# Optimization experiments

Measured on AMD Instinct MI355X. Metric: run time of the kernel, lower is better.

The kernel has to match this reference:

```python
import jax, jax.numpy as jnp
import numpy as np

B, T, IN, H, OUT = 4096, 28, 28, 1024, 10


def setup_inputs() -> dict:
    key = jax.random.key(0)
    ks = jax.random.split(key, 6)
    s_ih = 1.0 / np.sqrt(IN)
    s_h = 1.0 / np.sqrt(H)
    return {
        "x": jax.random.normal(ks[0], (B, T, IN), dtype=jnp.float32),
        "W_ih": jax.random.uniform(ks[1], (IN, 4 * H), jnp.float32, -s_ih, s_ih),
        "W_hh": jax.random.uniform(ks[2], (H, 4 * H), jnp.float32, -s_h, s_h),
        "b": jax.random.uniform(ks[3], (4 * H,), jnp.float32, -s_h, s_h),
        "Wc": jax.random.uniform(ks[4], (H, OUT), jnp.float32, -s_h, s_h),
        "bc": jax.random.uniform(ks[5], (OUT,), jnp.float32, -s_h, s_h),
    }


def _lstm_last_hidden(x, W_ih, W_hh, b):
    # Precompute input projections for all timesteps: [T, B, 4H]
    xg = jnp.einsum('bti,ig->tbg', x, W_ih) + b
    h0 = jnp.zeros((x.shape[0], W_hh.shape[0]), x.dtype)
    c0 = jnp.zeros_like(h0)

    def step(carry, xg_t):
        h, c = carry
        gates = xg_t + h @ W_hh  # [B, 4H]
        i, f, g, o = jnp.split(gates, 4, axis=-1)
        i = jax.nn.sigmoid(i)
        f = jax.nn.sigmoid(f)
        g = jnp.tanh(g)
        o = jax.nn.sigmoid(o)
        c = f * c + i * g
        h = o * jnp.tanh(c)
        return (h, c), None

    (h, _), _ = jax.lax.scan(step, (h0, c0), xg)
    return h


def reference(x, W_ih, W_hh, b, Wc, bc):
    h = _lstm_last_hidden(x, W_ih, W_hh, b)
    # dropout is identity at inference (eval mode)
    return h @ Wc + bc
```

## Files before the change

kernel.cpp:

```cpp
#include <hip/hip_runtime.h>
#include <hip/hip_fp16.h>
#include <stdint.h>

#define GLOBAL_AS __attribute__((address_space(1)))
#define LDS_AS    __attribute__((address_space(3)))

typedef __attribute__((ext_vector_type(8))) short  short8;
typedef __attribute__((ext_vector_type(4))) float  floatx4;

static constexpr int B_   = 4096;
static constexpr int T_   = 28;
static constexpr int IN_  = 28;
static constexpr int H_   = 1024;
static constexpr int G4_  = 4096;
static constexpr int OUT_ = 10;
static constexpr int NT_  = 16;

__device__ __forceinline__ float bf2f(unsigned short u) {
  union { uint32_t i; float f; } v; v.i = ((uint32_t)u) << 16; return v.f;
}
__device__ __forceinline__ unsigned short f2bf(float f) {
  union { float f; uint32_t i; } v; v.f = f;
  uint32_t x = v.i;
  uint32_t lsb = (x >> 16) & 1u;
  x += 0x7fffu + lsb;
  return (unsigned short)(x >> 16);
}
__device__ __forceinline__ float sigm(float x) {
  return __builtin_amdgcn_rcpf(1.f + __builtin_amdgcn_exp2f(-1.4426950408889634f * x));
}
__device__ __forceinline__ float tanh_f(float x) {
  return 1.f - 2.f * __builtin_amdgcn_rcpf(1.f + __builtin_amdgcn_exp2f(2.8853900817779268f * x));
}
__device__ __forceinline__ void stage16(const unsigned short* g, unsigned short* l) {
  __builtin_amdgcn_global_load_lds(
      (const GLOBAL_AS uint32_t*)g, (LDS_AS uint32_t*)l, 16, 0, 0);
}

__global__ __launch_bounds__(256) void conv_x_kernel(const float* __restrict__ x,
                                                     unsigned short* __restrict__ xb) {
  int row = blockIdx.x * 256 + threadIdx.x;
  int t  = row >> 12;
  int bb = row & 4095;
  const float* src = x + (bb * T_ + t) * IN_;
  unsigned short* dst = xb + row * 32;
#pragma unroll
  for (int k = 0; k < IN_; ++k) dst[k] = f2bf(src[k]);
  dst[28] = 0; dst[29] = 0; dst[30] = 0; dst[31] = 0;
}

__global__ __launch_bounds__(256) void perm_whh_kernel(const float* __restrict__ whh,
                                                       unsigned short* __restrict__ wp) {
  __shared__ float lds[64][17];
  int g64  = blockIdx.x >> 2;
  int gate = blockIdx.x & 3;
  int oc0  = gate * H_ + g64 * 16;
  int n0   = g64 * 64 + gate * 16;
  int tid  = threadIdx.x;
  for (int kc = 0; kc < 16; ++kc) {
    int k0 = kc * 64;
    __syncthreads();
#pragma unroll
    for (int e = 0; e < 4; ++e) {
      int idx = e * 256 + tid;
      int k = idx >> 4, cc = idx & 15;
      lds[k][cc] = whh[(k0 + k) * G4_ + oc0 + cc];
    }
    __syncthreads();
#pragma unroll
    for (int e = 0; e < 4; ++e) {
      int idx = e * 256 + tid;
      int n = idx >> 6, kk = idx & 63;
      wp[(n0 + n) * H_ + k0 + kk] = f2bf(lds[kk][n]);
    }
  }
}

__global__ __launch_bounds__(256) void perm_wih_kernel(const float* __restrict__ wih,
                                                       unsigned short* __restrict__ wip) {
  __shared__ float lds[28][17];
  int g64  = blockIdx.x >> 2;
  int gate = blockIdx.x & 3;
  int oc0  = gate * H_ + g64 * 16;
  int n0   = g64 * 64 + gate * 16;
  int tid  = threadIdx.x;
  for (int idx = tid; idx < 448; idx += 256) {
    int k = idx >> 4, cc = idx & 15;
    lds[k][cc] = wih[k * G4_ + oc0 + cc];
  }
  __syncthreads();
#pragma unroll
  for (int e = 0; e < 2; ++e) {
    int idx = e * 256 + tid;
    int n = idx >> 5, kk = idx & 31;
    wip[(n0 + n) * 32 + kk] = (kk < IN_) ? f2bf(lds[kk][n]) : (unsigned short)0;
  }
}

__global__ __launch_bounds__(512, 4) void lstm_step_kernel(
    const unsigned short* __restrict__ hprev,
    const unsigned short* __restrict__ wp,
    const unsigned short* __restrict__ xbt,
    const unsigned short* __restrict__ wip,
    const float* __restrict__ bias,
    unsigned short* __restrict__ cst,
    unsigned short* __restrict__ hnext,
    int first) {
  __shared__ __align__(16) unsigned short lds[24576];

  const int tid = threadIdx.x;
  const int w   = tid >> 6;
  const int l   = tid & 63;
  const int wm  = w >> 1;
  const int wn  = w & 1;
  const int lc  = l & 15;
  const int lk  = l >> 4;

  const int hid = blockIdx.x;
  const int xcd = hid & 7, q = hid >> 3;
  const int bx  = (xcd & 1) * 8 + (q & 7);
  const int by  = (xcd >> 1) * 8 + (q >> 3);
  const int m0  = bx * 256;
  const int n0  = by * 128;

  const int swz  = (lc & 7) << 4;
  const int swzx = (lc & 3) << 4;

  const int r8  = tid >> 3;
  const int c8  = (tid & 7) * 8;
  const int c8s = c8 ^ ((r8 & 7) * 8);
  const int rx   = tid >> 2;
  const int cx8s = ((tid & 3) * 8) ^ ((rx & 3) * 8);

  auto stageA = [&](int kt, int i) {
    stage16(hprev + (size_t)(m0 + i * 64 + r8) * H_ + kt * 64 + c8s,
            lds + i * 4096 + tid * 8);
  };
  auto stageB = [&](int kt, int j) {
    stage16(wp + (size_t)(n0 + j * 64 + r8) * H_ + kt * 64 + c8s,
            lds + 16384 + j * 4096 + tid * 8);
  };
  auto stageXA = [&](int half) {
    stage16(xbt + (size_t)(m0 + half * 128 + rx) * 32 + cx8s,
            lds + half * 4096 + tid * 8);
  };
  auto stageXB = [&]() {
    stage16(wip + (size_t)(n0 + rx) * 32 + cx8s,
            lds + 8192 + tid * 8);
  };
  auto ldsr = [&](int byteoff) -> short8 {
    return *reinterpret_cast<const short8*>(reinterpret_cast<const char*>(lds) + byteoff);
  };

  floatx4 acc[4][4];
#pragma unroll
  for (int i = 0; i < 4; ++i)
#pragma unroll
    for (int j = 0; j < 4; ++j) acc[i][j] = (floatx4){0.f, 0.f, 0.f, 0.f};

  short8 a[4][2];
  short8 b[2][2];

#define LOAD_A                                                                       \
  _Pragma("unroll") for (int m_ = 0; m_ < 4; ++m_)                                   \
  _Pragma("unroll") for (int k_ = 0; k_ < 2; ++k_)                                   \
    a[m_][k_] = ldsr((wm * 64 + m_ * 16 + lc) * 128 + ((k_ * 64 + lk * 16) ^ swz));

#define LOAD_B(P)                                                                    \
  _Pragma("unroll") for (int n_ = 0; n_ < 2; ++n_)                                   \
  _Pragma("unroll") for (int k_ = 0; k_ < 2; ++k_)                                   \
    b[n_][k_] = ldsr(32768 + (wn * 64 + ((P) * 2 + n_) * 16 + lc) * 128 +            \
                     ((k_ * 64 + lk * 16) ^ swz));

#define MFMA_P(P)                                                                    \
  __builtin_amdgcn_s_setprio(1);                                                     \
  _Pragma("unroll") for (int m_ = 0; m_ < 4; ++m_)                                   \
  _Pragma("unroll") for (int n_ = 0; n_ < 2; ++n_)                                   \
  _Pragma("unroll") for (int k_ = 0; k_ < 2; ++k_)                                   \
    acc[m_][(P) * 2 + n_] = __builtin_amdgcn_mfma_f32_16x16x32_bf16(                 \
        a[m_][k_], b[n_][k_], acc[m_][(P) * 2 + n_], 0, 0, 0);                       \
  __builtin_amdgcn_s_setprio(0);

#define BAR_ONLY                                                                     \
  __builtin_amdgcn_sched_barrier(0);                                                 \
  __builtin_amdgcn_s_barrier();                                                      \
  __builtin_amdgcn_sched_barrier(0);

#define BAR_VM0                                                                      \
  __builtin_amdgcn_sched_barrier(0);                                                 \
  asm volatile("s_waitcnt vmcnt(0)" ::: "memory");                                   \
  __builtin_amdgcn_s_barrier();                                                      \
  __builtin_amdgcn_sched_barrier(0);

  stageXA(0); stageXA(1); stageXB();
  BAR_VM0
  {
    short8 xb4[4];
#pragma unroll
    for (int nf = 0; nf < 4; ++nf)
      xb4[nf] = ldsr(16384 + (wn * 64 + nf * 16 + lc) * 64 + ((lk * 16) ^ swzx));
    __builtin_amdgcn_s_setprio(1);
#pragma unroll
    for (int mf = 0; mf < 4; ++mf) {
      short8 xa = ldsr((wm * 64 + mf * 16 + lc) * 64 + ((lk * 16) ^ swzx));
#pragma unroll
      for (int nf = 0; nf < 4; ++nf)
        acc[mf][nf] = __builtin_amdgcn_mfma_f32_16x16x32_bf16(xa, xb4[nf], acc[mf][nf], 0, 0, 0);
    }
    __builtin_amdgcn_s_setprio(0);
  }

  if (!first) {
    BAR_ONLY
#pragma unroll
    for (int i = 0; i < 4; ++i) stageA(0, i);
    stageB(0, 0); stageB(0, 1);
    BAR_VM0
    for (int kt = 0; kt < NT_; ++kt) {
      LOAD_A
      LOAD_B(0)
      MFMA_P(0)
      LOAD_B(1)
      MFMA_P(1)
      if (kt + 1 < NT_) {
        BAR_ONLY
#pragma unroll
        for (int i = 0; i < 4; ++i) stageA(kt + 1, i);
        stageB(kt + 1, 0); stageB(kt + 1, 1);
        BAR_VM0
      }
    }
  }

  const int jj  = (by * 2 + wn) * 16 + lc;
  const float bi  = bias[jj];
  const float bf_ = bias[H_ + jj];
  const float bg_ = bias[2 * H_ + jj];
  const float bo_ = bias[3 * H_ + jj];
#pragma unroll
  for (int mf = 0; mf < 4; ++mf) {
    const int rbase = m0 + wm * 64 + mf * 16 + lk * 4;
#pragma unroll
    for (int r = 0; r < 4; ++r) {
      const size_t idx = (size_t)(rbase + r) * H_ + jj;
      float ig = sigm(acc[mf][0][r] + bi);
      float fg = sigm(acc[mf][1][r] + bf_);
      float gg = tanh_f(acc[mf][2][r] + bg_);
      float og = sigm(acc[mf][3][r] + bo_);
      float cp = first ? 0.f : __half2float(__ushort_as_half(cst[idx]));
      float cn = fg * cp + ig * gg;
      cst[idx] = __half_as_ushort(__float2half(cn));
      hnext[idx] = f2bf(og * tanh_f(cn));
    }
  }
#undef LOAD_A
#undef LOAD_B
#undef MFMA_P
#undef BAR_ONLY
#undef BAR_VM0
}

__global__ __launch_bounds__(256) void cls_kernel(const unsigned short* __restrict__ h,
                                                  const float* __restrict__ wc,
                                                  const float* __restrict__ bc,
                                                  float* __restrict__ out) {
  int w = threadIdx.x >> 6, l = threadIdx.x & 63;
  int row = blockIdx.x * 4 + w;
  float acc[OUT_];
#pragma unroll
  for (int o = 0; o < OUT_; ++o) acc[o] = 0.f;
  const unsigned short* hr = h + row * H_;
  for (int k = l; k < H_; k += 64) {
    float hv = bf2f(hr[k]);
#pragma unroll
    for (int o = 0; o < OUT_; ++o) acc[o] += hv * wc[k * OUT_ + o];
  }
#pragma unroll
  for (int o = 0; o < OUT_; ++o) {
    float v = acc[o];
#pragma unroll
    for (int s = 32; s > 0; s >>= 1) v += __shfl_down(v, s, 64);
    if (l == 0) out[row * OUT_ + o] = v + bc[o];
  }
}

extern "C" void kernel_launch(void* const* d_in, const int* in_sizes, int n_in,
                              void* d_out, int out_size, void* d_ws, size_t ws_size,
                              hipStream_t stream) {
  const float* x    = (const float*)d_in[0];
  const float* wih  = (const float*)d_in[1];
  const float* whh  = (const float*)d_in[2];
  const float* bias = (const float*)d_in[3];
  const float* wc   = (const float*)d_in[4];
  const float* bc   = (const float*)d_in[5];
  float* out = (float*)d_out;

  char* ws = (char*)d_ws;
  unsigned short* wp  = (unsigned short*)(ws);
  unsigned short* wip = (unsigned short*)(ws + 8388608);
  unsigned short* xb  = (unsigned short*)(ws + 8650752);
  unsigned short* h0  = (unsigned short*)(ws + 15990784);
  unsigned short* h1  = (unsigned short*)(ws + 24379392);
  unsigned short* cst = (unsigned short*)(ws + 32768000);

  hipLaunchKernelGGL(conv_x_kernel,  dim3(448), dim3(256), 0, stream, x, xb);
  hipLaunchKernelGGL(perm_whh_kernel, dim3(256), dim3(256), 0, stream, whh, wp);
  hipLaunchKernelGGL(perm_wih_kernel, dim3(256), dim3(256), 0, stream, wih, wip);

  unsigned short* hb[2] = {h0, h1};
  for (int t = 0; t < T_; ++t) {
    unsigned short* hn = hb[t & 1];
    unsigned short* hp = hb[(t & 1) ^ 1];
    hipLaunchKernelGGL(lstm_step_kernel, dim3(512), dim3(512), 0, stream,
                       hp, wp, xb + (size_t)t * (B_ * 32), wip, bias, cst, hn,
                       (t == 0) ? 1 : 0);
  }
  hipLaunchKernelGGL(cls_kernel, dim3(1024), dim3(256), 0, stream, hb[1], wc, bc, out);
}
```

Measured before the change: 1.066 ms.

## Triple-buffer recurrent GEMM K-loop with async prefetch two tiles ahead

Restructures the per-step recurrent GEMM main loop from a single-buffered 64-wide K tile, which waited for all loads before every compute phase, into a 32-wide K tile with three LDS buffers. Global-to-LDS staging for tile k+2 is issued while tile k is computed, and partial vmcnt waits replace full drains. This hides global load latency behind MFMA work, at the cost of more LDS (72KB), which may reduce occupancy, and twice as many barriers per K.

```diff
diff --git a/kernel.cpp b/kernel.cpp
--- a/kernel.cpp
+++ b/kernel.cpp
@@ -14,7 +14,7 @@
 static constexpr int H_   = 1024;
 static constexpr int G4_  = 4096;
 static constexpr int OUT_ = 10;
-static constexpr int NT_  = 16;
+static constexpr int NK_  = 32;
 
 __device__ __forceinline__ float bf2f(unsigned short u) {
   union { uint32_t i; float f; } v; v.i = ((uint32_t)u) << 16; return v.f;
@@ -106,7 +106,7 @@
     unsigned short* __restrict__ cst,
     unsigned short* __restrict__ hnext,
     int first) {
-  __shared__ __align__(16) unsigned short lds[24576];
+  __shared__ __align__(16) unsigned short lds[36864];
 
   const int tid = threadIdx.x;
   const int w   = tid >> 6;
@@ -123,30 +123,24 @@
   const int m0  = bx * 256;
   const int n0  = by * 128;
 
-  const int swz  = (lc & 7) << 4;
-  const int swzx = (lc & 3) << 4;
-
-  const int r8  = tid >> 3;
-  const int c8  = (tid & 7) * 8;
-  const int c8s = c8 ^ ((r8 & 7) * 8);
-  const int rx   = tid >> 2;
-  const int cx8s = ((tid & 3) * 8) ^ ((rx & 3) * 8);
-
-  auto stageA = [&](int kt, int i) {
-    stage16(hprev + (size_t)(m0 + i * 64 + r8) * H_ + kt * 64 + c8s,
-            lds + i * 4096 + tid * 8);
-  };
-  auto stageB = [&](int kt, int j) {
-    stage16(wp + (size_t)(n0 + j * 64 + r8) * H_ + kt * 64 + c8s,
-            lds + 16384 + j * 4096 + tid * 8);
-  };
-  auto stageXA = [&](int half) {
-    stage16(xbt + (size_t)(m0 + half * 128 + rx) * 32 + cx8s,
-            lds + half * 4096 + tid * 8);
+  const int sl = (lk * 16) ^ (((lc >> 1) & 3) << 4);
+
+  const int r4 = tid >> 2;
+  const int cs = ((tid & 3) * 8) ^ (((r4 >> 1) & 3) * 8);
+
+  auto stageA = [&](int bufU, int kt, int i) {
+    stage16(hprev + (size_t)(m0 + i * 128 + r4) * H_ + kt * 32 + cs,
+            lds + bufU + i * 4096 + tid * 8);
+  };
+  auto stageB = [&](int bufU, int kt) {
+    stage16(wp + (size_t)(n0 + r4) * H_ + kt * 32 + cs,
+            lds + bufU + 8192 + tid * 8);
+  };
+  auto stageXA = [&](int i) {
+    stage16(xbt + (size_t)(m0 + i * 128 + r4) * 32 + cs, lds + i * 4096 + tid * 8);
   };
   auto stageXB = [&]() {
-    stage16(wip + (size_t)(n0 + rx) * 32 + cx8s,
-            lds + 8192 + tid * 8);
+    stage16(wip + (size_t)(n0 + r4) * 32 + cs, lds + 8192 + tid * 8);
   };
   auto ldsr = [&](int byteoff) -> short8 {
     return *reinterpret_cast<const short8*>(reinterpret_cast<const char*>(lds) + byteoff);
@@ -158,78 +152,64 @@
 #pragma unroll
     for (int j = 0; j < 4; ++j) acc[i][j] = (floatx4){0.f, 0.f, 0.f, 0.f};
 
-  short8 a[4][2];
-  short8 b[2][2];
-
-#define LOAD_A                                                                       \
+  short8 a[4];
+  short8 b[4];
+
+#define LOAD_AB(PB)                                                                  \
   _Pragma("unroll") for (int m_ = 0; m_ < 4; ++m_)                                   \
-  _Pragma("unroll") for (int k_ = 0; k_ < 2; ++k_)                                   \
-    a[m_][k_] = ldsr((wm * 64 + m_ * 16 + lc) * 128 + ((k_ * 64 + lk * 16) ^ swz));
-
-#define LOAD_B(P)                                                                    \
-  _Pragma("unroll") for (int n_ = 0; n_ < 2; ++n_)                                   \
-  _Pragma("unroll") for (int k_ = 0; k_ < 2; ++k_)                                   \
-    b[n_][k_] = ldsr(32768 + (wn * 64 + ((P) * 2 + n_) * 16 + lc) * 128 +            \
-                     ((k_ * 64 + lk * 16) ^ swz));
-
-#define MFMA_P(P)                                                                    \
+    a[m_] = ldsr((PB) + (wm * 64 + m_ * 16 + lc) * 64 + sl);                         \
+  _Pragma("unroll") for (int n_ = 0; n_ < 4; ++n_)                                   \
+    b[n_] = ldsr((PB) + 16384 + (wn * 64 + n_ * 16 + lc) * 64 + sl);
+
+#define MFMA_T                                                                       \
   __builtin_amdgcn_s_setprio(1);                                                     \
   _Pragma("unroll") for (int m_ = 0; m_ < 4; ++m_)                                   \
-  _Pragma("unroll") for (int n_ = 0; n_ < 2; ++n_)                                   \
-  _Pragma("unroll") for (int k_ = 0; k_ < 2; ++k_)                                   \
-    acc[m_][(P) * 2 + n_] = __builtin_amdgcn_mfma_f32_16x16x32_bf16(                 \
-        a[m_][k_], b[n_][k_], acc[m_][(P) * 2 + n_], 0, 0, 0);                       \
+  _Pragma("unroll") for (int n_ = 0; n_ < 4; ++n_)                                   \
+    acc[m_][n_] = __builtin_amdgcn_mfma_f32_16x16x32_bf16(                           \
+        a[m_], b[n_], acc[m_][n_], 0, 0, 0);                                         \
   __builtin_amdgcn_s_setprio(0);
 
-#define BAR_ONLY                                                                     \
+#define BAR                                                                          \
   __builtin_amdgcn_sched_barrier(0);                                                 \
   __builtin_amdgcn_s_barrier();                                                      \
   __builtin_amdgcn_sched_barrier(0);
 
-#define BAR_VM0                                                                      \
-  __builtin_amdgcn_sched_barrier(0);                                                 \
-  asm volatile("s_waitcnt vmcnt(0)" ::: "memory");                                   \
-  __builtin_amdgcn_s_barrier();                                                      \
+#define WAITV(VM)                                                                    \
+  asm volatile("s_waitcnt vmcnt(" #VM ")" ::: "memory");                             \
   __builtin_amdgcn_sched_barrier(0);
 
-  stageXA(0); stageXA(1); stageXB();
-  BAR_VM0
-  {
-    short8 xb4[4];
-#pragma unroll
-    for (int nf = 0; nf < 4; ++nf)
-      xb4[nf] = ldsr(16384 + (wn * 64 + nf * 16 + lc) * 64 + ((lk * 16) ^ swzx));
-    __builtin_amdgcn_s_setprio(1);
-#pragma unroll
-    for (int mf = 0; mf < 4; ++mf) {
-      short8 xa = ldsr((wm * 64 + mf * 16 + lc) * 64 + ((lk * 16) ^ swzx));
-#pragma unroll
-      for (int nf = 0; nf < 4; ++nf)
-        acc[mf][nf] = __builtin_amdgcn_mfma_f32_16x16x32_bf16(xa, xb4[nf], acc[mf][nf], 0, 0, 0);
-    }
-    __builtin_amdgcn_s_setprio(0);
-  }
-
-  if (!first) {
-    BAR_ONLY
-#pragma unroll
-    for (int i = 0; i < 4; ++i) stageA(0, i);
-    stageB(0, 0); stageB(0, 1);
-    BAR_VM0
-    for (int kt = 0; kt < NT_; ++kt) {
-      LOAD_A
-      LOAD_B(0)
-      MFMA_P(0)
-      LOAD_B(1)
-      MFMA_P(1)
-      if (kt + 1 < NT_) {
-        BAR_ONLY
-#pragma unroll
-        for (int i = 0; i < 4; ++i) stageA(kt + 1, i);
-        stageB(kt + 1, 0); stageB(kt + 1, 1);
-        BAR_VM0
-      }
-    }
+  if (first) {
+    stageXA(0); stageXA(1); stageXB();
+    WAITV(0)
+    BAR
+    LOAD_AB(0)
+    MFMA_T
+  } else {
+    stageXA(0); stageXA(1); stageXB();
+    stageA(12288, 0, 0); stageA(12288, 0, 1); stageB(12288, 0);
+    stageA(24576, 1, 0); stageA(24576, 1, 1); stageB(24576, 1);
+    WAITV(6)
+    BAR
+    LOAD_AB(0)
+    MFMA_T
+
+#define ITER(KT, RDB, WRB)                                                           \
+    BAR                                                                              \
+    if ((KT) + 2 < NK_) {                                                            \
+      stageA((WRB), (KT) + 2, 0); stageA((WRB), (KT) + 2, 1); stageB((WRB), (KT) + 2); \
+      WAITV(6)                                                                       \
+    } else if ((KT) + 2 == NK_) { WAITV(3) } else { WAITV(0) }                       \
+    LOAD_AB((RDB) * 2)                                                               \
+    MFMA_T
+
+    for (int kt = 0; kt < 30; kt += 3) {
+      ITER(kt,     12288, 0)
+      ITER(kt + 1, 24576, 12288)
+      ITER(kt + 2, 0,     24576)
+    }
+    ITER(30, 12288, 0)
+    ITER(31, 24576, 12288)
+#undef ITER
   }
 
   const int jj  = (by * 2 + wn) * 16 + lc;
@@ -253,11 +233,10 @@
       hnext[idx] = f2bf(og * tanh_f(cn));
     }
   }
-#undef LOAD_A
-#undef LOAD_B
-#undef MFMA_P
-#undef BAR_ONLY
-#undef BAR_VM0
+#undef LOAD_AB
+#undef MFMA_T
+#undef BAR
+#undef WAITV
 }
 
 __global__ __launch_bounds__(256) void cls_kernel(const unsigned short* __restrict__ h,
```

After: 1.158 ms. 1.09x slower.

## Load recurrent A operand directly from global and double-buffer weight tiles in LDS

Applied to the files above, without the earlier changes.

The h_prev (A) fragments and the x-projection A fragments are now read straight from global memory into registers instead of being staged through LDS. The W_hh (B) tiles are double-buffered in LDS with a two-tile prefetch distance, using partial vmcnt waits. This is meant to overlap weight loads with MFMA work, remove the LDS staging traffic for A, and shrink LDS use from 48KB to 32KB so more blocks can be resident. The cost is that the A loads are not prefetched, so their global latency lands right before the MFMAs. A also loses the sharing between the two wn waves that LDS staging gave.

```diff
diff --git a/kernel.cpp b/kernel.cpp
--- a/kernel.cpp
+++ b/kernel.cpp
@@ -106,7 +106,7 @@
     unsigned short* __restrict__ cst,
     unsigned short* __restrict__ hnext,
     int first) {
-  __shared__ __align__(16) unsigned short lds[24576];
+  __shared__ __align__(16) unsigned short lds[16384];
 
   const int tid = threadIdx.x;
   const int w   = tid >> 6;
@@ -127,31 +127,24 @@
   const int swzx = (lc & 3) << 4;
 
   const int r8  = tid >> 3;
-  const int c8  = (tid & 7) * 8;
-  const int c8s = c8 ^ ((r8 & 7) * 8);
-  const int rx   = tid >> 2;
-  const int cx8s = ((tid & 3) * 8) ^ ((rx & 3) * 8);
-
-  auto stageA = [&](int kt, int i) {
-    stage16(hprev + (size_t)(m0 + i * 64 + r8) * H_ + kt * 64 + c8s,
-            lds + i * 4096 + tid * 8);
-  };
-  auto stageB = [&](int kt, int j) {
+  const int c8s = ((tid & 7) * 8) ^ ((r8 & 7) * 8);
+  const int rx  = tid >> 2;
+  const int cxs = ((tid & 3) * 8) ^ ((rx & 3) * 8);
+
+  auto stageB = [&](int bufU, int kt, int j) {
     stage16(wp + (size_t)(n0 + j * 64 + r8) * H_ + kt * 64 + c8s,
-            lds + 16384 + j * 4096 + tid * 8);
-  };
-  auto stageXA = [&](int half) {
-    stage16(xbt + (size_t)(m0 + half * 128 + rx) * 32 + cx8s,
-            lds + half * 4096 + tid * 8);
+            lds + bufU + j * 4096 + tid * 8);
   };
   auto stageXB = [&]() {
-    stage16(wip + (size_t)(n0 + rx) * 32 + cx8s,
-            lds + 8192 + tid * 8);
+    stage16(wip + (size_t)(n0 + rx) * 32 + cxs, lds + tid * 8);
   };
   auto ldsr = [&](int byteoff) -> short8 {
     return *reinterpret_cast<const short8*>(reinterpret_cast<const char*>(lds) + byteoff);
   };
 
+  const unsigned short* aRow = hprev + (size_t)(m0 + wm * 64 + lc) * H_ + lk * 8;
+  const unsigned short* xRow = xbt + (size_t)(m0 + wm * 64 + lc) * 32 + lk * 8;
+
   floatx4 acc[4][4];
 #pragma unroll
   for (int i = 0; i < 4; ++i)
@@ -161,15 +154,15 @@
   short8 a[4][2];
   short8 b[2][2];
 
-#define LOAD_A                                                                       \
+#define LOAD_A_DIR(KT)                                                               \
   _Pragma("unroll") for (int m_ = 0; m_ < 4; ++m_)                                   \
   _Pragma("unroll") for (int k_ = 0; k_ < 2; ++k_)                                   \
-    a[m_][k_] = ldsr((wm * 64 + m_ * 16 + lc) * 128 + ((k_ * 64 + lk * 16) ^ swz));
-
-#define LOAD_B(P)                                                                    \
+    a[m_][k_] = *reinterpret_cast<const short8*>(aRow + m_ * (16 * H_) + (KT) * 64 + k_ * 32);
+
+#define LOAD_B(BUFBYTE, P)                                                           \
   _Pragma("unroll") for (int n_ = 0; n_ < 2; ++n_)                                   \
   _Pragma("unroll") for (int k_ = 0; k_ < 2; ++k_)                                   \
-    b[n_][k_] = ldsr(32768 + (wn * 64 + ((P) * 2 + n_) * 16 + lc) * 128 +            \
+    b[n_][k_] = ldsr((BUFBYTE) + (wn * 64 + ((P) * 2 + n_) * 16 + lc) * 128 +        \
                      ((k_ * 64 + lk * 16) ^ swz));
 
 #define MFMA_P(P)                                                                    \
@@ -186,48 +179,65 @@
   __builtin_amdgcn_s_barrier();                                                      \
   __builtin_amdgcn_sched_barrier(0);
 
-#define BAR_VM0                                                                      \
+#define BAR_VM(VM)                                                                   \
   __builtin_amdgcn_sched_barrier(0);                                                 \
-  asm volatile("s_waitcnt vmcnt(0)" ::: "memory");                                   \
+  asm volatile("s_waitcnt vmcnt(" #VM ")" ::: "memory");                             \
   __builtin_amdgcn_s_barrier();                                                      \
   __builtin_amdgcn_sched_barrier(0);
 
-  stageXA(0); stageXA(1); stageXB();
-  BAR_VM0
-  {
+  if (first) {
+    stageXB();
+    BAR_VM(0)
     short8 xb4[4];
 #pragma unroll
     for (int nf = 0; nf < 4; ++nf)
-      xb4[nf] = ldsr(16384 + (wn * 64 + nf * 16 + lc) * 64 + ((lk * 16) ^ swzx));
+      xb4[nf] = ldsr((wn * 64 + nf * 16 + lc) * 64 + ((lk * 16) ^ swzx));
     __builtin_amdgcn_s_setprio(1);
 #pragma unroll
     for (int mf = 0; mf < 4; ++mf) {
-      short8 xa = ldsr((wm * 64 + mf * 16 + lc) * 64 + ((lk * 16) ^ swzx));
+      short8 xa = *reinterpret_cast<const short8*>(xRow + mf * (16 * 32));
 #pragma unroll
       for (int nf = 0; nf < 4; ++nf)
         acc[mf][nf] = __builtin_amdgcn_mfma_f32_16x16x32_bf16(xa, xb4[nf], acc[mf][nf], 0, 0, 0);
     }
     __builtin_amdgcn_s_setprio(0);
-  }
-
-  if (!first) {
+  } else {
+    stageXB();
+    stageB(8192, 0, 0); stageB(8192, 0, 1);
+    BAR_VM(2)
+    {
+      short8 xb4[4];
+#pragma unroll
+      for (int nf = 0; nf < 4; ++nf)
+        xb4[nf] = ldsr((wn * 64 + nf * 16 + lc) * 64 + ((lk * 16) ^ swzx));
+      __builtin_amdgcn_s_setprio(1);
+#pragma unroll
+      for (int mf = 0; mf < 4; ++mf) {
+        short8 xa = *reinterpret_cast<const short8*>(xRow + mf * (16 * 32));
+#pragma unroll
+        for (int nf = 0; nf < 4; ++nf)
+          acc[mf][nf] = __builtin_amdgcn_mfma_f32_16x16x32_bf16(xa, xb4[nf], acc[mf][nf], 0, 0, 0);
+      }
+      __builtin_amdgcn_s_setprio(0);
+    }
     BAR_ONLY
-#pragma unroll
-    for (int i = 0; i < 4; ++i) stageA(0, i);
-    stageB(0, 0); stageB(0, 1);
-    BAR_VM0
+    stageB(0, 1, 0); stageB(0, 1, 1);
+    BAR_VM(2)
     for (int kt = 0; kt < NT_; ++kt) {
-      LOAD_A
-      LOAD_B(0)
+      const int bufB = ((kt & 1) ^ 1) * 16384;
+      LOAD_A_DIR(kt)
+      LOAD_B(bufB, 0)
       MFMA_P(0)
-      LOAD_B(1)
+      LOAD_B(bufB, 1)
       MFMA_P(1)
       if (kt + 1 < NT_) {
         BAR_ONLY
-#pragma unroll
-        for (int i = 0; i < 4; ++i) stageA(kt + 1, i);
-        stageB(kt + 1, 0); stageB(kt + 1, 1);
-        BAR_VM0
+        if (kt + 2 < NT_) {
+          stageB(bufB / 2, kt + 2, 0); stageB(bufB / 2, kt + 2, 1);
+          BAR_VM(2)
+        } else {
+          BAR_VM(0)
+        }
       }
     }
   }
@@ -253,11 +263,11 @@
       hnext[idx] = f2bf(og * tanh_f(cn));
     }
   }
-#undef LOAD_A
+#undef LOAD_A_DIR
 #undef LOAD_B
 #undef MFMA_P
 #undef BAR_ONLY
-#undef BAR_VM0
+#undef BAR_VM
 }
 
 __global__ __launch_bounds__(256) void cls_kernel(const unsigned short* __restrict__ h,
```

Measured after the change: 2.147 ms. 2.01x slower.
